# Kernel optimization log

Hardware: AMD Instinct MI355X
Metric: run time of the kernel (lower is better)

Reference implementation:

```python
import jax, jax.numpy as jnp
import numpy as np
from jax import lax

KSIZE, STRIDE, RATE, FUSE_K, SCALE, FUSE = 3, 1, 2, 3, 10.0, True


def _same_pad(h, w, k, s):
    oh, ow = -(-h // s), -(-w // s)
    ph = max(0, (oh - 1) * s + k - h)
    pw = max(0, (ow - 1) * s + k - w)
    return (ph // 2, ph - ph // 2), (pw // 2, pw - pw // 2), oh, ow


def extract_patches(x, k, s):
    # x: [B,C,H,W] -> ([B, L, C, k, k], Ho, Wo); matches torch Unfold with 'same' padding
    B, C, H, W = x.shape
    (pt, pb), (pl, pr), Ho, Wo = _same_pad(H, W, k, s)
    xp = jnp.pad(x, ((0, 0), (0, 0), (pt, pb), (pl, pr)))
    rows = []
    for i in range(k):
        cols = [xp[:, :, i:i + s * (Ho - 1) + 1:s, j:j + s * (Wo - 1) + 1:s] for j in range(k)]
        rows.append(jnp.stack(cols, axis=2))  # [B,C,k,Ho,Wo]
    pat = jnp.stack(rows, axis=2)  # [B,C,k,k,Ho,Wo]
    pat = pat.reshape(B, C, k, k, Ho * Wo).transpose(0, 4, 1, 2, 3)
    return pat, Ho, Wo


def setup_inputs() -> dict:
    key = jax.random.key(0)
    kf, kb = jax.random.split(key)
    f = jax.random.normal(kf, (2, 128, 64, 64), dtype=jnp.float32)
    b = jax.random.normal(kb, (2, 128, 64, 64), dtype=jnp.float32)
    mask = jnp.zeros((2, 1, 256, 256), dtype=jnp.float32)
    return {"f": f, "b": b, "mask": mask}


def _forward(f, b, mask):
    B, C, Hr, Wr = f.shape
    kernel = 2 * RATE
    # raw background patches used as deconv kernels: [B, L, C, 4, 4]
    raw_w, _, _ = extract_patches(b, kernel, RATE * STRIDE)
    # nearest 1/rate downsample (torch nearest picks every rate-th pixel)
    fd = f[:, :, ::RATE, ::RATE]
    bd = b[:, :, ::RATE, ::RATE]
    Hf, Wf = fd.shape[2], fd.shape[3]
    Hb, Wb = bd.shape[2], bd.shape[3]
    L = Hb * Wb
    w, _, _ = extract_patches(bd, KSIZE, STRIDE)  # [B, L, C, 3, 3]
    # mask -> validity per background patch (original uses batch 0's mask only)
    md = mask[:, :, ::4 * RATE, ::4 * RATE]
    m, _, _ = extract_patches(md, KSIZE, STRIDE)  # [B, L, 1, 3, 3]
    mm = (jnp.mean(m[0], axis=(1, 2, 3)) == 0.0).astype(f.dtype)  # [L]
    # l2-normalize patch kernels (escape_NaN added per element before sum, as in torch)
    wn = w / jnp.sqrt(jnp.sum(w * w + 1e-4, axis=(2, 3, 4), keepdims=True))
    # correlation conv == batched GEMM over extracted foreground patches
    fp, _, _ = extract_patches(fd, KSIZE, 1)  # [B, P=Hf*Wf, C, 3, 3]
    scores = jnp.einsum('bpckl,bqckl->bqp', fp, wn)  # [B, L, Hf*Wf]
    scores = scores.reshape(B, Hb, Wb, Hf, Wf)

    if FUSE:
        def fuse_diag(y2):  # conv with 3x3 identity kernel, same pad == 3 diagonal shifts
            yp = jnp.pad(y2, ((1, 1), (1, 1)))
            return yp[:-2, :-2] + yp[1:-1, 1:-1] + yp[2:, 2:]

        def fuse_one(s):  # [Hb,Wb,Hf,Wf]
            y = fuse_diag(s.reshape(Hb * Wb, Hf * Wf)).reshape(Hb, Wb, Hf, Wf)
            y = y.transpose(1, 0, 3, 2)
            y = fuse_diag(y.reshape(Wb * Hb, Wf * Hf)).reshape(Wb, Hb, Wf, Hf)
            return y.transpose(1, 0, 3, 2)

        scores = jax.vmap(fuse_one)(scores)

    yi = scores.reshape(B, L, Hf, Wf) * mm[None, :, None, None]
    yi = jax.nn.softmax(yi * SCALE, axis=1) * mm[None, :, None, None]

    # transposed conv with per-batch raw patches as kernels (stride=rate, padding=1), /4
    def deconv_one(attn, wpat):  # attn [L,Hf,Wf], wpat [L,C,4,4]
        rhs = jnp.flip(wpat, axis=(2, 3)).transpose(1, 0, 2, 3)  # [C, L, 4, 4]
        pad = kernel - 1 - 1  # equivalent VALID padding for transposed conv with padding=1
        out = lax.conv_general_dilated(attn[None], rhs, (1, 1),
                                       padding=((pad, pad), (pad, pad)),
                                       lhs_dilation=(RATE, RATE),
                                       dimension_numbers=('NCHW', 'OIHW', 'NCHW'))
        return out[0] / 4.0

    y = jax.vmap(deconv_one)(yi, raw_w)  # [B, C, Hr, Wr]
    return y


def reference(f, b, mask):
    return _forward(f, b, mask)
```

## Files before the change

kernel.cpp:

```cpp
#include <hip/hip_runtime.h>
#include <hip/hip_bf16.h>
#include <math.h>

constexpr int HS = 32;
constexpr int Lq = 1024;
constexpr int CN = 128;

typedef short bf16x8 __attribute__((ext_vector_type(8)));
typedef float f32x4  __attribute__((ext_vector_type(4)));

__device__ inline unsigned short f2bf(float x) {
    union { float f; unsigned int u; } c; c.f = x;
    return (unsigned short)((c.u + 0x7FFF + ((c.u >> 16) & 1)) >> 16);
}
__device__ inline float bf2f(unsigned short h) {
    union { unsigned int u; float f; } c; c.u = ((unsigned int)h) << 16;
    return c.f;
}

__device__ inline void gload16(const void* g, void* l) {
    __builtin_amdgcn_global_load_lds(
        (const __attribute__((address_space(1))) unsigned int*)g,
        (__attribute__((address_space(3))) unsigned int*)l, 16, 0, 0);
}

__global__ __launch_bounds__(256) void k_prep3(const float* __restrict__ f,
                                               const float* __restrict__ bsrc,
                                               unsigned short* __restrict__ fH, unsigned short* __restrict__ fL,
                                               unsigned short* __restrict__ bH, unsigned short* __restrict__ bL,
                                               float* __restrict__ ssq,
                                               unsigned short* __restrict__ Wm) {
    int tx = threadIdx.x;
    if (blockIdx.x < 512) {
        int u = blockIdx.x * 4 + (tx >> 6);
        int lane = tx & 63;
        int p = u & (Lq - 1), bb = u >> 10;
        int py = p >> 5, px = p & 31;
        long srcbase = (((long)bb * CN) * 64 + 2 * py) * 64 + 2 * px;
        float s = 0.f;
#pragma unroll
        for (int i = 0; i < 2; ++i) {
            int c = lane + i * 64;
            long src = srcbase + (long)c * 4096;
            float fv = f[src], bv = bsrc[src];
            int o = u * CN + c;
            unsigned short fh = f2bf(fv), bh = f2bf(bv);
            fH[o] = fh; fL[o] = f2bf(fv - bf2f(fh));
            bH[o] = bh; bL[o] = f2bf(bv - bf2f(bh));
            s += bv * bv;
        }
        for (int off = 32; off > 0; off >>= 1) s += __shfl_down(s, off, 64);
        if (lane == 0) ssq[u] = s;
    } else {
        int idx = (blockIdx.x - 512) * 256 + tx;
        int q  = idx & (Lq - 1);
        int m  = (idx >> 10) & 2047;
        int bb = idx >> 21;
        int c = m >> 4, u = (m >> 2) & 3, v = m & 3;
        int qy = q >> 5, qx = q & 31;
        int y = 2 * qy + u - 1, x = 2 * qx + v - 1;
        float val = 0.f;
        if ((unsigned)y < 64u && (unsigned)x < 64u)
            val = bsrc[(((long)bb * CN + c) * 64 + y) * 64 + x];
        Wm[idx] = f2bf(val);
    }
}

__global__ __launch_bounds__(256) void k_nm(const float* __restrict__ ssq, const float* __restrict__ mask,
                                            float* __restrict__ norms, float* __restrict__ mmb) {
    int idx = blockIdx.x * 256 + threadIdx.x;
    if (idx < 2048) {
        int q = idx & (Lq - 1);
        int bb = idx >> 10;
        int qy = q >> 5, qx = q & 31;
        float s = 0.1152f;
        for (int dk = -1; dk <= 1; ++dk) {
            int y = qy + dk; if ((unsigned)y >= (unsigned)HS) continue;
            for (int dl = -1; dl <= 1; ++dl) {
                int x = qx + dl; if ((unsigned)x >= (unsigned)HS) continue;
                s += ssq[bb * Lq + y * HS + x];
            }
        }
        norms[idx] = sqrtf(s);
    } else {
        int q = idx - 2048;
        int qy = q >> 5, qx = q & 31;
        float s = 0.f;
        for (int dk = -1; dk <= 1; ++dk) {
            int y = qy + dk; if ((unsigned)y >= (unsigned)HS) continue;
            for (int dl = -1; dl <= 1; ++dl) {
                int x = qx + dl; if ((unsigned)x >= (unsigned)HS) continue;
                s += mask[(8 * y) * 256 + 8 * x];
            }
        }
        mmb[q] = (s == 0.0f) ? 1.0f : 0.0f;
    }
}

__global__ __launch_bounds__(256) void k_gram(const unsigned short* __restrict__ fH,
                                              const unsigned short* __restrict__ fL,
                                              const unsigned short* __restrict__ bH,
                                              const unsigned short* __restrict__ bL,
                                              float* __restrict__ GT) {
    const long bz = blockIdx.z;
    const unsigned short* AH = fH + bz * 131072;
    const unsigned short* AL = fL + bz * 131072;
    const unsigned short* BH = bH + bz * 131072;
    const unsigned short* BL = bL + bz * 131072;
    float* C = GT + (bz << 20);
    int t = threadIdx.x, w = t >> 6, lane = t & 63, quad = lane >> 4, l16 = lane & 15;
    int wm = blockIdx.x * 64 + (w & 1) * 32;
    int wn = blockIdx.y * 64 + (w >> 1) * 32;
    int ko = quad * 8;
    f32x4 acc[2][2] = {};
#pragma unroll
    for (int k0 = 0; k0 < 128; k0 += 32) {
        bf16x8 ah0 = *(const bf16x8*)&AH[(wm + l16) * 128 + ko + k0];
        bf16x8 ah1 = *(const bf16x8*)&AH[(wm + 16 + l16) * 128 + ko + k0];
        bf16x8 al0 = *(const bf16x8*)&AL[(wm + l16) * 128 + ko + k0];
        bf16x8 al1 = *(const bf16x8*)&AL[(wm + 16 + l16) * 128 + ko + k0];
        bf16x8 bh0 = *(const bf16x8*)&BH[(wn + l16) * 128 + ko + k0];
        bf16x8 bh1 = *(const bf16x8*)&BH[(wn + 16 + l16) * 128 + ko + k0];
        bf16x8 bl0 = *(const bf16x8*)&BL[(wn + l16) * 128 + ko + k0];
        bf16x8 bl1 = *(const bf16x8*)&BL[(wn + 16 + l16) * 128 + ko + k0];
        acc[0][0] = __builtin_amdgcn_mfma_f32_16x16x32_bf16(ah0, bh0, acc[0][0], 0, 0, 0);
        acc[0][1] = __builtin_amdgcn_mfma_f32_16x16x32_bf16(ah0, bh1, acc[0][1], 0, 0, 0);
        acc[1][0] = __builtin_amdgcn_mfma_f32_16x16x32_bf16(ah1, bh0, acc[1][0], 0, 0, 0);
        acc[1][1] = __builtin_amdgcn_mfma_f32_16x16x32_bf16(ah1, bh1, acc[1][1], 0, 0, 0);
        acc[0][0] = __builtin_amdgcn_mfma_f32_16x16x32_bf16(ah0, bl0, acc[0][0], 0, 0, 0);
        acc[0][1] = __builtin_amdgcn_mfma_f32_16x16x32_bf16(ah0, bl1, acc[0][1], 0, 0, 0);
        acc[1][0] = __builtin_amdgcn_mfma_f32_16x16x32_bf16(ah1, bl0, acc[1][0], 0, 0, 0);
        acc[1][1] = __builtin_amdgcn_mfma_f32_16x16x32_bf16(ah1, bl1, acc[1][1], 0, 0, 0);
        acc[0][0] = __builtin_amdgcn_mfma_f32_16x16x32_bf16(al0, bh0, acc[0][0], 0, 0, 0);
        acc[0][1] = __builtin_amdgcn_mfma_f32_16x16x32_bf16(al0, bh1, acc[0][1], 0, 0, 0);
        acc[1][0] = __builtin_amdgcn_mfma_f32_16x16x32_bf16(al1, bh0, acc[1][0], 0, 0, 0);
        acc[1][1] = __builtin_amdgcn_mfma_f32_16x16x32_bf16(al1, bh1, acc[1][1], 0, 0, 0);
    }
#pragma unroll
    for (int i = 0; i < 2; ++i)
#pragma unroll
        for (int j = 0; j < 2; ++j) {
            int mrow = wm + i * 16 + quad * 4;
            int ncol = wn + j * 16 + l16;
#pragma unroll
            for (int r = 0; r < 4; ++r)
                C[(long)(mrow + r) * Lq + ncol] = acc[i][j][r];
        }
}

__global__ __launch_bounds__(256) void k_s0T(const float* __restrict__ GT, const float* __restrict__ norms,
                                             float* __restrict__ S0T) {
    int idx = blockIdx.x * 256 + threadIdx.x;
    int q  = idx & (Lq - 1);
    int pp = (idx >> 10) & (Lq - 1);
    int bb = idx >> 20;
    int qy = q >> 5, qx = q & 31, py = pp >> 5, px = pp & 31;
    const float* Gb = GT + ((long)bb << 20);
    float s = 0.f;
#pragma unroll
    for (int dk = -1; dk <= 1; ++dk) {
        if ((unsigned)(qy + dk) >= (unsigned)HS || (unsigned)(py + dk) >= (unsigned)HS) continue;
#pragma unroll
        for (int dl = -1; dl <= 1; ++dl) {
            if ((unsigned)(qx + dl) >= (unsigned)HS || (unsigned)(px + dl) >= (unsigned)HS) continue;
            int sft = dk * HS + dl;
            s += Gb[(long)(pp + sft) * Lq + (q + sft)];
        }
    }
    S0T[idx] = s / norms[bb * Lq + q];
}

__global__ __launch_bounds__(256) void k_fuse12(const float* __restrict__ S0, float* __restrict__ S2) {
    int idx = blockIdx.x * 256 + threadIdx.x;
    int p  = idx & (Lq - 1);
    int q  = (idx >> 10) & (Lq - 1);
    int bb = idx >> 20;
    int hb = q >> 5, wb = q & 31, hf = p >> 5, wf = p & 31;
    int ip = wb * HS + hb, jp = wf * HS + hf;
    const float* S = S0 + (long)bb * Lq * Lq;
    float s = 0.f;
#pragma unroll
    for (int d = -1; d <= 1; ++d) {
        int t = ip + d, r = jp + d;
        if ((unsigned)t < (unsigned)Lq && (unsigned)r < (unsigned)Lq) {
            int q2 = (t & 31) * HS + (t >> 5);
            int p2 = (r & 31) * HS + (r >> 5);
            long base = (long)q2 * Lq + p2;
            float v = S[base];
            if (q2 > 0 && p2 > 0)             v += S[base - (Lq + 1)];
            if (q2 < Lq - 1 && p2 < Lq - 1)   v += S[base + (Lq + 1)];
            s += v;
        }
    }
    S2[idx] = s;
}

__global__ __launch_bounds__(256) void k_softmaxT(const float* __restrict__ S2T, const float* __restrict__ mmb,
                                                  unsigned short* __restrict__ At) {
    int wid = blockIdx.x * 4 + (threadIdx.x >> 6);
    int lane = threadIdx.x & 63;
    int bb = wid >> 10, p = wid & (Lq - 1);
    const float* row = S2T + ((long)bb << 20) + (long)p * Lq;
    unsigned short* orow = At + ((long)bb << 20) + (long)p * Lq;
    float x[16]; float mx = -1e30f;
#pragma unroll
    for (int i = 0; i < 16; ++i) {
        int q = i * 64 + lane;
        x[i] = row[q] * mmb[q] * 10.0f;
        mx = fmaxf(mx, x[i]);
    }
    for (int off = 32; off > 0; off >>= 1) mx = fmaxf(mx, __shfl_xor(mx, off, 64));
    float e[16]; float s = 0.f;
#pragma unroll
    for (int i = 0; i < 16; ++i) { e[i] = __expf(x[i] - mx); s += e[i]; }
    for (int off = 32; off > 0; off >>= 1) s += __shfl_xor(s, off, 64);
    float inv = 1.0f / s;
#pragma unroll
    for (int i = 0; i < 16; ++i) {
        int q = i * 64 + lane;
        orow[q] = f2bf(e[i] * mmb[q] * inv);
    }
}

__global__ __launch_bounds__(256) void k_gemm_mfma(const unsigned short* __restrict__ WmA,
                                                   const unsigned short* __restrict__ At,
                                                   float* __restrict__ Cm) {
    const long bz = blockIdx.z;
    const unsigned short* A = WmA + bz * (2048L * Lq);
    const unsigned short* B = At  + bz * ((long)Lq * Lq);
    float* C = Cm + bz * (2048L * Lq);
    __shared__ __align__(16) unsigned short As[128 * 64];
    __shared__ __align__(16) unsigned short Bs[64 * 64];
    int t = threadIdx.x;
    int w = t >> 6, lane = t & 63, quad = lane >> 4, l16 = lane & 15;
    int wr = w >> 1, wc = w & 1;
    int m0 = blockIdx.x * 128, n0 = blockIdx.y * 64;
    int srow = t >> 3;
    int scol = (t & 7) * 8;
    f32x4 acc[4][2] = {};
    for (int k0 = 0; k0 < Lq; k0 += 64) {
        __syncthreads();
#pragma unroll
        for (int r = 0; r < 4; ++r)
            gload16(A + (long)(m0 + r * 32 + srow) * Lq + k0 + scol,
                    &As[(r * 32 + srow) * 64 + scol]);
#pragma unroll
        for (int r = 0; r < 2; ++r)
            gload16(B + (long)(n0 + r * 32 + srow) * Lq + k0 + scol,
                    &Bs[(r * 32 + srow) * 64 + scol]);
        __syncthreads();
#pragma unroll
        for (int ks = 0; ks < 2; ++ks) {
            bf16x8 a[4], b[2];
#pragma unroll
            for (int i = 0; i < 4; ++i)
                a[i] = *(const bf16x8*)&As[(wr * 64 + i * 16 + l16) * 64 + ks * 32 + quad * 8];
#pragma unroll
            for (int j = 0; j < 2; ++j)
                b[j] = *(const bf16x8*)&Bs[(wc * 32 + j * 16 + l16) * 64 + ks * 32 + quad * 8];
#pragma unroll
            for (int i = 0; i < 4; ++i)
#pragma unroll
                for (int j = 0; j < 2; ++j)
                    acc[i][j] = __builtin_amdgcn_mfma_f32_16x16x32_bf16(a[i], b[j], acc[i][j], 0, 0, 0);
        }
    }
#pragma unroll
    for (int i = 0; i < 4; ++i) {
        int mrow = m0 + wr * 64 + i * 16 + quad * 4;
#pragma unroll
        for (int j = 0; j < 2; ++j) {
            int ncol = n0 + wc * 32 + j * 16 + l16;
#pragma unroll
            for (int r = 0; r < 4; ++r)
                C[(long)(mrow + r) * Lq + ncol] = acc[i][j][r];
        }
    }
}

__global__ __launch_bounds__(256) void k_epi2(const float* __restrict__ P, float* __restrict__ out) {
    int idx = blockIdx.x * 256 + threadIdx.x;
    int ox = idx & 63, oy = (idx >> 6) & 63, c = (idx >> 12) & 127, bb = idx >> 19;
    const float* Pb = P + (long)bb * 2048 * Lq;
    float s = 0.f;
#pragma unroll
    for (int u = 0; u < 4; ++u) {
        int t = oy + u - 2;
        if (t & 1) continue;
        int iy = t >> 1;
        if ((unsigned)iy >= (unsigned)HS) continue;
#pragma unroll
        for (int v = 0; v < 4; ++v) {
            int r = ox + v - 2;
            if (r & 1) continue;
            int ix = r >> 1;
            if ((unsigned)ix >= (unsigned)HS) continue;
            s += Pb[(long)((c << 4) + (3 - u) * 4 + (3 - v)) * Lq + (iy << 5) + ix];
        }
    }
    out[idx] = 0.25f * s;
}

extern "C" void kernel_launch(void* const* d_in, const int* in_sizes, int n_in,
                              void* d_out, int out_size, void* d_ws, size_t ws_size,
                              hipStream_t stream) {
    const float* f    = (const float*)d_in[0];
    const float* bsrc = (const float*)d_in[1];
    const float* mask = (const float*)d_in[2];
    float* out = (float*)d_out;
    float* ws = (float*)d_ws;

    float* ssq   = ws;
    float* norms = ssq   + 2048;
    float* mmb   = norms + 2048;
    unsigned short* fH = (unsigned short*)(mmb + 1024);
    unsigned short* fL = fH + 262144;
    unsigned short* bH = fL + 262144;
    unsigned short* bL = bH + 262144;
    float* GTa   = (float*)(bL + 262144);
    float* C1    = GTa + 2097152;
    float* C2    = C1  + 2097152;
    unsigned short* Wm = (unsigned short*)(C2 + 2097152);
    float* S0T  = C1;
    float* S2T  = C2;
    unsigned short* attnT = (unsigned short*)GTa;
    float* P    = C1;

    hipLaunchKernelGGL(k_prep3,     dim3(16896),      dim3(256), 0, stream, f, bsrc, fH, fL, bH, bL, ssq, Wm);
    hipLaunchKernelGGL(k_nm,        dim3(12),         dim3(256), 0, stream, ssq, mask, norms, mmb);
    hipLaunchKernelGGL(k_gram,      dim3(16, 16, 2),  dim3(256), 0, stream, fH, fL, bH, bL, GTa);
    hipLaunchKernelGGL(k_s0T,       dim3(8192),       dim3(256), 0, stream, GTa, norms, S0T);
    hipLaunchKernelGGL(k_fuse12,    dim3(8192),       dim3(256), 0, stream, S0T, S2T);
    hipLaunchKernelGGL(k_softmaxT,  dim3(512),        dim3(256), 0, stream, S2T, mmb, attnT);
    hipLaunchKernelGGL(k_gemm_mfma, dim3(16, 16, 2),  dim3(256), 0, stream, Wm, attnT, P);
    hipLaunchKernelGGL(k_epi2,      dim3(4096),       dim3(256), 0, stream, P, out);
}
```

Baseline: 144.0 us.

## Fuse deconv epilogue into GEMM via atomics and merge small kernels

The col2im epilogue kernel is removed. The GEMM now scatters its scaled accumulators directly into the output with atomicAdd, after the output is zeroed in extra blocks of the prep kernel. The norm/mask kernel is folded into an extra z-slice of the gram kernel. Together these drop two launches and the round trip of the large P intermediate through memory, at the cost of float atomic contention and nondeterministic summation order.

```diff
diff --git a/kernel.cpp b/kernel.cpp
--- a/kernel.cpp
+++ b/kernel.cpp
@@ -29,7 +29,8 @@
                                                unsigned short* __restrict__ fH, unsigned short* __restrict__ fL,
                                                unsigned short* __restrict__ bH, unsigned short* __restrict__ bL,
                                                float* __restrict__ ssq,
-                                               unsigned short* __restrict__ Wm) {
+                                               unsigned short* __restrict__ Wm,
+                                               float* __restrict__ out) {
     int tx = threadIdx.x;
     if (blockIdx.x < 512) {
         int u = blockIdx.x * 4 + (tx >> 6);
@@ -51,7 +52,7 @@
         }
         for (int off = 32; off > 0; off >>= 1) s += __shfl_down(s, off, 64);
         if (lane == 0) ssq[u] = s;
-    } else {
+    } else if (blockIdx.x < 16896) {
         int idx = (blockIdx.x - 512) * 256 + tx;
         int q  = idx & (Lq - 1);
         int m  = (idx >> 10) & 2047;
@@ -63,37 +64,10 @@
         if ((unsigned)y < 64u && (unsigned)x < 64u)
             val = bsrc[(((long)bb * CN + c) * 64 + y) * 64 + x];
         Wm[idx] = f2bf(val);
-    }
-}
-
-__global__ __launch_bounds__(256) void k_nm(const float* __restrict__ ssq, const float* __restrict__ mask,
-                                            float* __restrict__ norms, float* __restrict__ mmb) {
-    int idx = blockIdx.x * 256 + threadIdx.x;
-    if (idx < 2048) {
-        int q = idx & (Lq - 1);
-        int bb = idx >> 10;
-        int qy = q >> 5, qx = q & 31;
-        float s = 0.1152f;
-        for (int dk = -1; dk <= 1; ++dk) {
-            int y = qy + dk; if ((unsigned)y >= (unsigned)HS) continue;
-            for (int dl = -1; dl <= 1; ++dl) {
-                int x = qx + dl; if ((unsigned)x >= (unsigned)HS) continue;
-                s += ssq[bb * Lq + y * HS + x];
-            }
-        }
-        norms[idx] = sqrtf(s);
     } else {
-        int q = idx - 2048;
-        int qy = q >> 5, qx = q & 31;
-        float s = 0.f;
-        for (int dk = -1; dk <= 1; ++dk) {
-            int y = qy + dk; if ((unsigned)y >= (unsigned)HS) continue;
-            for (int dl = -1; dl <= 1; ++dl) {
-                int x = qx + dl; if ((unsigned)x >= (unsigned)HS) continue;
-                s += mask[(8 * y) * 256 + 8 * x];
-            }
-        }
-        mmb[q] = (s == 0.0f) ? 1.0f : 0.0f;
+        int idx = (blockIdx.x - 16896) * 256 + tx;
+        float4 z = {0.f, 0.f, 0.f, 0.f};
+        *(float4*)&out[(long)idx << 2] = z;
     }
 }
 
@@ -101,7 +75,41 @@
                                               const unsigned short* __restrict__ fL,
                                               const unsigned short* __restrict__ bH,
                                               const unsigned short* __restrict__ bL,
-                                              float* __restrict__ GT) {
+                                              float* __restrict__ GT,
+                                              const float* __restrict__ ssq, const float* __restrict__ mask,
+                                              float* __restrict__ norms, float* __restrict__ mmb) {
+    if (blockIdx.z == 2) {
+        int blk = blockIdx.y * 16 + blockIdx.x;
+        if (blk >= 12) return;
+        int idx = blk * 256 + threadIdx.x;
+        if (idx < 2048) {
+            int q = idx & (Lq - 1);
+            int bb = idx >> 10;
+            int qy = q >> 5, qx = q & 31;
+            float s = 0.1152f;
+            for (int dk = -1; dk <= 1; ++dk) {
+                int y = qy + dk; if ((unsigned)y >= (unsigned)HS) continue;
+                for (int dl = -1; dl <= 1; ++dl) {
+                    int x = qx + dl; if ((unsigned)x >= (unsigned)HS) continue;
+                    s += ssq[bb * Lq + y * HS + x];
+                }
+            }
+            norms[idx] = sqrtf(s);
+        } else if (idx < 3072) {
+            int q = idx - 2048;
+            int qy = q >> 5, qx = q & 31;
+            float s = 0.f;
+            for (int dk = -1; dk <= 1; ++dk) {
+                int y = qy + dk; if ((unsigned)y >= (unsigned)HS) continue;
+                for (int dl = -1; dl <= 1; ++dl) {
+                    int x = qx + dl; if ((unsigned)x >= (unsigned)HS) continue;
+                    s += mask[(8 * y) * 256 + 8 * x];
+                }
+            }
+            mmb[q] = (s == 0.0f) ? 1.0f : 0.0f;
+        }
+        return;
+    }
     const long bz = blockIdx.z;
     const unsigned short* AH = fH + bz * 131072;
     const unsigned short* AL = fL + bz * 131072;
@@ -224,11 +232,10 @@
 
 __global__ __launch_bounds__(256) void k_gemm_mfma(const unsigned short* __restrict__ WmA,
                                                    const unsigned short* __restrict__ At,
-                                                   float* __restrict__ Cm) {
+                                                   float* __restrict__ out) {
     const long bz = blockIdx.z;
     const unsigned short* A = WmA + bz * (2048L * Lq);
     const unsigned short* B = At  + bz * ((long)Lq * Lq);
-    float* C = Cm + bz * (2048L * Lq);
     __shared__ __align__(16) unsigned short As[128 * 64];
     __shared__ __align__(16) unsigned short Bs[64 * 64];
     int t = threadIdx.x;
@@ -265,40 +272,25 @@
                     acc[i][j] = __builtin_amdgcn_mfma_f32_16x16x32_bf16(a[i], b[j], acc[i][j], 0, 0, 0);
         }
     }
+    float* ob = out + ((long)bz << 19);
 #pragma unroll
     for (int i = 0; i < 4; ++i) {
-        int mrow = m0 + wr * 64 + i * 16 + quad * 4;
+        int c = (m0 + wr * 64 + i * 16) >> 4;
 #pragma unroll
         for (int j = 0; j < 2; ++j) {
             int ncol = n0 + wc * 32 + j * 16 + l16;
-#pragma unroll
-            for (int r = 0; r < 4; ++r)
-                C[(long)(mrow + r) * Lq + ncol] = acc[i][j][r];
-        }
-    }
-}
-
-__global__ __launch_bounds__(256) void k_epi2(const float* __restrict__ P, float* __restrict__ out) {
-    int idx = blockIdx.x * 256 + threadIdx.x;
-    int ox = idx & 63, oy = (idx >> 6) & 63, c = (idx >> 12) & 127, bb = idx >> 19;
-    const float* Pb = P + (long)bb * 2048 * Lq;
-    float s = 0.f;
-#pragma unroll
-    for (int u = 0; u < 4; ++u) {
-        int t = oy + u - 2;
-        if (t & 1) continue;
-        int iy = t >> 1;
-        if ((unsigned)iy >= (unsigned)HS) continue;
-#pragma unroll
-        for (int v = 0; v < 4; ++v) {
-            int r = ox + v - 2;
-            if (r & 1) continue;
-            int ix = r >> 1;
-            if ((unsigned)ix >= (unsigned)HS) continue;
-            s += Pb[(long)((c << 4) + (3 - u) * 4 + (3 - v)) * Lq + (iy << 5) + ix];
-        }
-    }
-    out[idx] = 0.25f * s;
+            int iy = ncol >> 5, ix = ncol & 31;
+            int oy = 2 * iy + quad - 1;
+            if ((unsigned)oy >= 64u) continue;
+            float* orow = ob + ((long)c * 64 + oy) * 64;
+#pragma unroll
+            for (int r = 0; r < 4; ++r) {
+                int ox = 2 * ix + r - 1;
+                if ((unsigned)ox < 64u)
+                    atomicAdd(&orow[ox], 0.25f * acc[i][j][r]);
+            }
+        }
+    }
 }
 
 extern "C" void kernel_launch(void* const* d_in, const int* in_sizes, int n_in,
@@ -324,14 +316,11 @@
     float* S0T  = C1;
     float* S2T  = C2;
     unsigned short* attnT = (unsigned short*)GTa;
-    float* P    = C1;
-
-    hipLaunchKernelGGL(k_prep3,     dim3(16896),      dim3(256), 0, stream, f, bsrc, fH, fL, bH, bL, ssq, Wm);
-    hipLaunchKernelGGL(k_nm,        dim3(12),         dim3(256), 0, stream, ssq, mask, norms, mmb);
-    hipLaunchKernelGGL(k_gram,      dim3(16, 16, 2),  dim3(256), 0, stream, fH, fL, bH, bL, GTa);
+
+    hipLaunchKernelGGL(k_prep3,     dim3(17920),      dim3(256), 0, stream, f, bsrc, fH, fL, bH, bL, ssq, Wm, out);
+    hipLaunchKernelGGL(k_gram,      dim3(16, 16, 3),  dim3(256), 0, stream, fH, fL, bH, bL, GTa, ssq, mask, norms, mmb);
     hipLaunchKernelGGL(k_s0T,       dim3(8192),       dim3(256), 0, stream, GTa, norms, S0T);
     hipLaunchKernelGGL(k_fuse12,    dim3(8192),       dim3(256), 0, stream, S0T, S2T);
     hipLaunchKernelGGL(k_softmaxT,  dim3(512),        dim3(256), 0, stream, S2T, mmb, attnT);
-    hipLaunchKernelGGL(k_gemm_mfma, dim3(16, 16, 2),  dim3(256), 0, stream, Wm, attnT, P);
-    hipLaunchKernelGGL(k_epi2,      dim3(4096),       dim3(256), 0, stream, P, out);
-}
+    hipLaunchKernelGGL(k_gemm_mfma, dim3(16, 16, 2),  dim3(256), 0, stream, Wm, attnT, out);
+}
```

Measured after the change: 155.0 us. 1.08x slower.

## Double-buffer GEMM LDS tiles with XOR swizzle and merge norm kernel into gram

Applied to the files above, without the earlier changes.

The attention-by-patches GEMM now keeps two LDS buffers, so the global-to-LDS load of the next K tile is issued before the MFMAs on the current tile. This cuts the loop to one barrier per iteration. LDS columns are XOR-swizzled by row to reduce bank conflicts on the bf16x8 reads. The small norm/mask kernel becomes an extra z-slice of the gram launch, removing one kernel launch. The cost is doubled LDS use per block, which may lower occupancy.

```diff
diff --git a/kernel.cpp b/kernel.cpp
--- a/kernel.cpp
+++ b/kernel.cpp
@@ -66,42 +66,45 @@
     }
 }
 
-__global__ __launch_bounds__(256) void k_nm(const float* __restrict__ ssq, const float* __restrict__ mask,
-                                            float* __restrict__ norms, float* __restrict__ mmb) {
-    int idx = blockIdx.x * 256 + threadIdx.x;
-    if (idx < 2048) {
-        int q = idx & (Lq - 1);
-        int bb = idx >> 10;
-        int qy = q >> 5, qx = q & 31;
-        float s = 0.1152f;
-        for (int dk = -1; dk <= 1; ++dk) {
-            int y = qy + dk; if ((unsigned)y >= (unsigned)HS) continue;
-            for (int dl = -1; dl <= 1; ++dl) {
-                int x = qx + dl; if ((unsigned)x >= (unsigned)HS) continue;
-                s += ssq[bb * Lq + y * HS + x];
-            }
-        }
-        norms[idx] = sqrtf(s);
-    } else {
-        int q = idx - 2048;
-        int qy = q >> 5, qx = q & 31;
-        float s = 0.f;
-        for (int dk = -1; dk <= 1; ++dk) {
-            int y = qy + dk; if ((unsigned)y >= (unsigned)HS) continue;
-            for (int dl = -1; dl <= 1; ++dl) {
-                int x = qx + dl; if ((unsigned)x >= (unsigned)HS) continue;
-                s += mask[(8 * y) * 256 + 8 * x];
-            }
-        }
-        mmb[q] = (s == 0.0f) ? 1.0f : 0.0f;
-    }
-}
-
 __global__ __launch_bounds__(256) void k_gram(const unsigned short* __restrict__ fH,
                                               const unsigned short* __restrict__ fL,
                                               const unsigned short* __restrict__ bH,
                                               const unsigned short* __restrict__ bL,
-                                              float* __restrict__ GT) {
+                                              float* __restrict__ GT,
+                                              const float* __restrict__ ssq, const float* __restrict__ mask,
+                                              float* __restrict__ norms, float* __restrict__ mmb) {
+    if (blockIdx.z == 2) {
+        int blk = blockIdx.y * 16 + blockIdx.x;
+        if (blk >= 12) return;
+        int idx = blk * 256 + threadIdx.x;
+        if (idx < 2048) {
+            int q = idx & (Lq - 1);
+            int bb = idx >> 10;
+            int qy = q >> 5, qx = q & 31;
+            float s = 0.1152f;
+            for (int dk = -1; dk <= 1; ++dk) {
+                int y = qy + dk; if ((unsigned)y >= (unsigned)HS) continue;
+                for (int dl = -1; dl <= 1; ++dl) {
+                    int x = qx + dl; if ((unsigned)x >= (unsigned)HS) continue;
+                    s += ssq[bb * Lq + y * HS + x];
+                }
+            }
+            norms[idx] = sqrtf(s);
+        } else if (idx < 3072) {
+            int q = idx - 2048;
+            int qy = q >> 5, qx = q & 31;
+            float s = 0.f;
+            for (int dk = -1; dk <= 1; ++dk) {
+                int y = qy + dk; if ((unsigned)y >= (unsigned)HS) continue;
+                for (int dl = -1; dl <= 1; ++dl) {
+                    int x = qx + dl; if ((unsigned)x >= (unsigned)HS) continue;
+                    s += mask[(8 * y) * 256 + 8 * x];
+                }
+            }
+            mmb[q] = (s == 0.0f) ? 1.0f : 0.0f;
+        }
+        return;
+    }
     const long bz = blockIdx.z;
     const unsigned short* AH = fH + bz * 131072;
     const unsigned short* AL = fL + bz * 131072;
@@ -229,42 +232,54 @@
     const unsigned short* A = WmA + bz * (2048L * Lq);
     const unsigned short* B = At  + bz * ((long)Lq * Lq);
     float* C = Cm + bz * (2048L * Lq);
-    __shared__ __align__(16) unsigned short As[128 * 64];
-    __shared__ __align__(16) unsigned short Bs[64 * 64];
+    __shared__ __align__(16) unsigned short As[2][128 * 64];
+    __shared__ __align__(16) unsigned short Bs[2][64 * 64];
     int t = threadIdx.x;
     int w = t >> 6, lane = t & 63, quad = lane >> 4, l16 = lane & 15;
     int wr = w >> 1, wc = w & 1;
     int m0 = blockIdx.x * 128, n0 = blockIdx.y * 64;
-    int srow = t >> 3;
-    int scol = (t & 7) * 8;
+    int srow  = t >> 3;
+    int scolS = ((t & 7) ^ ((t >> 3) & 7)) << 3;
+    int sdst  = t * 8;
+    int xr    = l16 & 7;
     f32x4 acc[4][2] = {};
+
+#define STAGE(buf, kk) do {                                                         \
+    _Pragma("unroll")                                                               \
+    for (int r = 0; r < 4; ++r)                         \
+        gload16(A + (long)(m0 + r * 32 + srow) * Lq + (kk) + scolS,                 \
+                &As[buf][r * 2048 + sdst]);                                         \
+    _Pragma("unroll")                                                               \
+    for (int r = 0; r < 2; ++r)                          \
+        gload16(B + (long)(n0 + r * 32 + srow) * Lq + (kk) + scolS,                 \
+                &Bs[buf][r * 2048 + sdst]);                                         \
+} while (0)
+
+    int cur = 0;
+    STAGE(0, 0);
+    __syncthreads();
     for (int k0 = 0; k0 < Lq; k0 += 64) {
-        __syncthreads();
-#pragma unroll
-        for (int r = 0; r < 4; ++r)
-            gload16(A + (long)(m0 + r * 32 + srow) * Lq + k0 + scol,
-                    &As[(r * 32 + srow) * 64 + scol]);
-#pragma unroll
-        for (int r = 0; r < 2; ++r)
-            gload16(B + (long)(n0 + r * 32 + srow) * Lq + k0 + scol,
-                    &Bs[(r * 32 + srow) * 64 + scol]);
-        __syncthreads();
+        if (k0 + 64 < Lq) STAGE(cur ^ 1, k0 + 64);
 #pragma unroll
         for (int ks = 0; ks < 2; ++ks) {
+            int slot = ((ks * 4 + quad) ^ xr) << 3;
             bf16x8 a[4], b[2];
 #pragma unroll
             for (int i = 0; i < 4; ++i)
-                a[i] = *(const bf16x8*)&As[(wr * 64 + i * 16 + l16) * 64 + ks * 32 + quad * 8];
+                a[i] = *(const bf16x8*)&As[cur][(wr * 64 + i * 16 + l16) * 64 + slot];
 #pragma unroll
             for (int j = 0; j < 2; ++j)
-                b[j] = *(const bf16x8*)&Bs[(wc * 32 + j * 16 + l16) * 64 + ks * 32 + quad * 8];
+                b[j] = *(const bf16x8*)&Bs[cur][(wc * 32 + j * 16 + l16) * 64 + slot];
 #pragma unroll
             for (int i = 0; i < 4; ++i)
 #pragma unroll
                 for (int j = 0; j < 2; ++j)
                     acc[i][j] = __builtin_amdgcn_mfma_f32_16x16x32_bf16(a[i], b[j], acc[i][j], 0, 0, 0);
         }
-    }
+        __syncthreads();
+        cur ^= 1;
+    }
+#undef STAGE
 #pragma unroll
     for (int i = 0; i < 4; ++i) {
         int mrow = m0 + wr * 64 + i * 16 + quad * 4;
@@ -327,8 +342,7 @@
     float* P    = C1;
 
     hipLaunchKernelGGL(k_prep3,     dim3(16896),      dim3(256), 0, stream, f, bsrc, fH, fL, bH, bL, ssq, Wm);
-    hipLaunchKernelGGL(k_nm,        dim3(12),         dim3(256), 0, stream, ssq, mask, norms, mmb);
-    hipLaunchKernelGGL(k_gram,      dim3(16, 16, 2),  dim3(256), 0, stream, fH, fL, bH, bL, GTa);
+    hipLaunchKernelGGL(k_gram,      dim3(16, 16, 3),  dim3(256), 0, stream, fH, fL, bH, bL, GTa, ssq, mask, norms, mmb);
     hipLaunchKernelGGL(k_s0T,       dim3(8192),       dim3(256), 0, stream, GTa, norms, S0T);
     hipLaunchKernelGGL(k_fuse12,    dim3(8192),       dim3(256), 0, stream, S0T, S2T);
     hipLaunchKernelGGL(k_softmaxT,  dim3(512),        dim3(256), 0, stream, S2T, mmb, attnT);
```

After: 138.8 us. 3.6% less time.
